# Performance work log

Measured on AMD Instinct MI355X. Metric: run time of the kernel, lower is better.

## Reference

```python
import jax, jax.numpy as jnp
import numpy as np

D = 128   # d_model
K = 128   # knn neighbors
NL = 4    # point transformer layers
EPS = 1e-5


def _timestep_embedding(t, dim):
    half = dim // 2
    freqs = jnp.exp(-jnp.log(10000.0) * jnp.arange(half, dtype=jnp.float32) / (half - 1))
    args = t.astype(jnp.float32)[:, None] * freqs[None, :]          # [B, half]
    return jnp.concatenate([jnp.sin(args), jnp.cos(args)], axis=-1)  # [B, dim]


def _layernorm(x, g, b):
    m = jnp.mean(x, axis=-1, keepdims=True)
    v = jnp.mean((x - m) ** 2, axis=-1, keepdims=True)
    return (x - m) / jnp.sqrt(v + EPS) * g + b


def _pt_layer(xyz, feat, Wq, bq, Wk, bk, Wv, bv, Wp1, bp1, Wp2, bp2, gamma, Wpr, bpr):
    # full pairwise squared distance [B,N,N]
    sq = jnp.sum(xyz * xyz, axis=-1)
    dist = sq[:, :, None] + sq[:, None, :] - 2.0 * jnp.einsum('bnd,bmd->bnm', xyz, xyz)
    _, idx = jax.lax.top_k(-dist, K)                 # k smallest -> [B,N,K]
    gather = jax.vmap(lambda p, i: p[i])             # per-batch gather along N
    nxyz = gather(xyz, idx)                          # [B,N,K,3]
    nfeat = gather(feat, idx)                        # [B,N,K,D]
    q = (feat @ Wq + bq)[:, :, None, :]              # [B,N,1,D]
    k = nfeat @ Wk + bk                              # [B,N,K,D]
    v = nfeat @ Wv + bv                              # [B,N,K,D]
    rel = xyz[:, :, None, :] - nxyz                  # [B,N,K,3]
    pe = jax.nn.relu(rel @ Wp1 + bp1) @ Wp2 + bp2    # [B,N,K,D]
    attn = jax.nn.softmax(jnp.sum(q - k + pe, axis=-1, keepdims=True), axis=-2)  # over K
    agg = jnp.sum(attn * (v + pe), axis=2)           # [B,N,D]
    return feat + gamma * (agg @ Wpr + bpr)


def reference(xyz, feat, x_t, t,
              pt_Wq, pt_bq, pt_Wk, pt_bk, pt_Wv, pt_bv,
              pt_Wp1, pt_bp1, pt_Wp2, pt_bp2, pt_gamma, pt_Wproj, pt_bproj,
              tW1, tb1, tW2, tb2,
              nW1, nb1, ng1, nbeta1, nW2, nb2, ng2, nbeta2, nW3, nb3):
    fused = feat
    for i in range(NL):
        fused = _pt_layer(xyz, fused,
                          pt_Wq[i], pt_bq[i], pt_Wk[i], pt_bk[i], pt_Wv[i], pt_bv[i],
                          pt_Wp1[i], pt_bp1[i], pt_Wp2[i], pt_bp2[i],
                          pt_gamma[i], pt_Wproj[i], pt_bproj[i])
    # DDPM head
    temb = _timestep_embedding(t, D)                 # [B,D]
    temb = jax.nn.relu(temb @ tW1 + tb1) @ tW2 + tb2
    temb = jnp.broadcast_to(temb[:, None, :], fused.shape[:2] + (D,))
    h = jnp.concatenate([x_t, fused, temb], axis=-1)  # [B,N,3+2D]
    h = jax.nn.relu(_layernorm(h @ nW1 + nb1, ng1, nbeta1))
    h = jax.nn.relu(_layernorm(h @ nW2 + nb2, ng2, nbeta2))
    return h @ nW3 + nb3                              # [B,N,3]


def setup_inputs() -> dict:
    key = jax.random.key(0)
    ks = jax.random.split(key, 32)
    B, N = 2, 2048
    rn = lambda k, shape, s=0.02: (jax.random.normal(k, shape) * s).astype(jnp.float32)
    in_dim = 3 + D + D
    return {
        'xyz': jax.random.normal(ks[0], (B, N, 3), dtype=jnp.float32),
        'feat': jax.random.normal(ks[1], (B, N, D), dtype=jnp.float32),
        'x_t': jax.random.normal(ks[2], (B, N, 3), dtype=jnp.float32),
        't': jax.random.randint(ks[3], (B,), 0, 1000),
        'pt_Wq': rn(ks[4], (NL, D, D)), 'pt_bq': jnp.zeros((NL, D), jnp.float32),
        'pt_Wk': rn(ks[5], (NL, D, D)), 'pt_bk': jnp.zeros((NL, D), jnp.float32),
        'pt_Wv': rn(ks[6], (NL, D, D)), 'pt_bv': jnp.zeros((NL, D), jnp.float32),
        'pt_Wp1': rn(ks[7], (NL, 3, D)), 'pt_bp1': jnp.zeros((NL, D), jnp.float32),
        'pt_Wp2': rn(ks[8], (NL, D, D)), 'pt_bp2': jnp.zeros((NL, D), jnp.float32),
        'pt_gamma': rn(ks[9], (NL,), 0.1),
        'pt_Wproj': rn(ks[10], (NL, D, D)), 'pt_bproj': jnp.zeros((NL, D), jnp.float32),
        'tW1': rn(ks[11], (D, D)), 'tb1': jnp.zeros((D,), jnp.float32),
        'tW2': rn(ks[12], (D, D)), 'tb2': jnp.zeros((D,), jnp.float32),
        'nW1': rn(ks[13], (in_dim, D)), 'nb1': jnp.zeros((D,), jnp.float32),
        'ng1': jnp.ones((D,), jnp.float32), 'nbeta1': jnp.zeros((D,), jnp.float32),
        'nW2': rn(ks[14], (D, D)), 'nb2': jnp.zeros((D,), jnp.float32),
        'ng2': jnp.ones((D,), jnp.float32), 'nbeta2': jnp.zeros((D,), jnp.float32),
        'nW3': rn(ks[15], (D, 3)), 'nb3': jnp.zeros((3,), jnp.float32),
    }
```

## Files before the change

### kernel.cpp

```cpp
#include <hip/hip_runtime.h>
#include <math.h>

#define B_SZ 2
#define N_PTS 2048
#define DM 128
#define KNN 128
#define NLAYER 4
#define ROWS (B_SZ * N_PTS)
#define RBV 4
#define EPSLN 1e-5f

__device__ __forceinline__ float waveSum(float v) {
#pragma unroll
  for (int o = 32; o > 0; o >>= 1) v += __shfl_xor(v, o, 64);
  return v;
}
__device__ __forceinline__ float waveMax(float v) {
#pragma unroll
  for (int o = 32; o > 0; o >>= 1) v = fmaxf(v, __shfl_xor(v, o, 64));
  return v;
}
__device__ __forceinline__ float blockSum128(float v, float* s2, int t) {
  float w = waveSum(v);
  __syncthreads();
  if ((t & 63) == 0) s2[t >> 6] = w;
  __syncthreads();
  return s2[0] + s2[1];
}
__device__ __forceinline__ unsigned waveScanIncl(unsigned v, int lane) {
#pragma unroll
  for (int o = 1; o < 64; o <<= 1) {
    unsigned u = (unsigned)__shfl_up((int)v, o, 64);
    if (lane >= o) v += u;
  }
  return v;
}

__global__ __launch_bounds__(256) void knn_kernel(const float* __restrict__ xyz,
                                                  int* __restrict__ idx) {
  int row = blockIdx.x;
  int b = row >> 11, i = row & (N_PTS - 1);
  const float* xb = xyz + (size_t)b * N_PTS * 3;
  int tid = threadIdx.x;
  int lane = tid & 63, wid = tid >> 6;

  __shared__ unsigned hist[256];
  __shared__ unsigned wred[4];
  __shared__ unsigned sel[2];

  float xi = xb[i * 3 + 0], yi = xb[i * 3 + 1], zi = xb[i * 3 + 2];
  float sqi = xi * xi + yi * yi + zi * zi;

  float p[24];
  {
    const float4* xb4 = (const float4*)xb;
#pragma unroll
    for (int q = 0; q < 6; ++q) {
      float4 v = xb4[tid * 6 + q];
      p[q * 4 + 0] = v.x; p[q * 4 + 1] = v.y; p[q * 4 + 2] = v.z; p[q * 4 + 3] = v.w;
    }
  }
  unsigned key[8];
#pragma unroll
  for (int s = 0; s < 8; ++s) {
    float xj = p[s * 3 + 0], yj = p[s * 3 + 1], zj = p[s * 3 + 2];
    float d = sqi + xj * xj + yj * yj + zj * zj -
              2.0f * (xi * xj + yi * yj + zi * zj);
    unsigned u = __float_as_uint(d);
    key[s] = (u & 0x80000000u) ? ~u : (u | 0x80000000u);
  }

  unsigned prefix = 0;
  unsigned need = KNN;
  for (int shift = 24; shift >= 0; shift -= 8) {
    hist[tid] = 0;
    __syncthreads();
    if (shift == 24) {
#pragma unroll
      for (int s = 0; s < 8; ++s) {
        unsigned bin = key[s] >> 24;
        unsigned long long act = __ballot(1);
        while (act) {
          int src = __builtin_ctzll(act);
          unsigned bsel = (unsigned)__shfl((int)bin, src, 64);
          unsigned long long grp = __ballot(bin == bsel);
          if (lane == src)
            atomicAdd(&hist[bsel], (unsigned)__builtin_popcountll(grp));
          act &= ~grp;
        }
      }
    } else {
#pragma unroll
      for (int s = 0; s < 8; ++s) {
        unsigned k = key[s];
        if ((k >> (shift + 8)) == prefix)
          atomicAdd(&hist[(k >> shift) & 255u], 1u);
      }
    }
    __syncthreads();
    unsigned h = hist[tid];
    unsigned incl = waveScanIncl(h, lane);
    if (lane == 63) wred[wid] = incl;
    __syncthreads();
    unsigned offs = 0;
    for (int w = 0; w < wid; ++w) offs += wred[w];
    incl += offs;
    unsigned excl = incl - h;
    if (excl < need && need <= incl) { sel[0] = (unsigned)tid; sel[1] = need - excl; }
    __syncthreads();
    prefix = (prefix << 8) | sel[0];
    need = sel[1];
  }
  unsigned T = prefix;
  int need_eq = (int)need;

  unsigned clt = 0, ceq = 0;
#pragma unroll
  for (int s = 0; s < 8; ++s) {
    clt += (key[s] < T);
    ceq += (key[s] == T);
  }
  unsigned packed = clt | (ceq << 16);
  unsigned incl = waveScanIncl(packed, lane);
  if (lane == 63) wred[wid] = incl;
  __syncthreads();
  unsigned offs = 0;
  for (int w = 0; w < wid; ++w) offs += wred[w];
  unsigned totAll = wred[0] + wred[1] + wred[2] + wred[3];
  incl += offs;
  unsigned excl = incl - packed;
  int lt_base = (int)(excl & 0xFFFFu);
  int eq_base = (int)(excl >> 16);
  int total_lt = (int)(totAll & 0xFFFFu);

  int* orow = idx + (size_t)row * KNN;
  int lpos = 0, epos = 0;
#pragma unroll
  for (int s = 0; s < 8; ++s) {
    int j = tid * 8 + s;
    unsigned k = key[s];
    if (k < T) {
      orow[lt_base + lpos] = j; lpos++;
    } else if (k == T) {
      int r = eq_base + epos; epos++;
      if (r < need_eq) orow[total_lt + r] = j;
    }
  }
}

__global__ __launch_bounds__(128) void prep_kernel(
    const float* __restrict__ Wq, const float* __restrict__ bq,
    const float* __restrict__ Wk, const float* __restrict__ bk,
    const float* __restrict__ Wp2, const float* __restrict__ bp2,
    float* __restrict__ rs, float* __restrict__ ssum,
    const int* __restrict__ t, const float* __restrict__ tW1,
    const float* __restrict__ tb1, const float* __restrict__ tW2,
    const float* __restrict__ tb2, float* __restrict__ temb) {
  int blk = blockIdx.x, d = threadIdx.x;
  __shared__ float s2[2];
  __shared__ float emb[DM];
  __shared__ float h1[DM];
  if (blk < NLAYER) {
    int l = blk;
    const float* wq = Wq + (size_t)l * DM * DM;
    const float* wk = Wk + (size_t)l * DM * DM;
    const float* wp2 = Wp2 + (size_t)l * DM * DM;
    float a = 0.f, b = 0.f, c = 0.f;
    for (int j = 0; j < DM; ++j) {
      a += wq[d * DM + j];
      b += wk[d * DM + j];
      c += wp2[d * DM + j];
    }
    rs[l * 3 * DM + d] = a;
    rs[l * 3 * DM + DM + d] = b;
    rs[l * 3 * DM + 2 * DM + d] = c;
    float sq = blockSum128(bq[l * DM + d], s2, d);
    float sk = blockSum128(bk[l * DM + d], s2, d);
    float sp = blockSum128(bp2[l * DM + d], s2, d);
    if (d == 0) { ssum[l * 4 + 0] = sq; ssum[l * 4 + 1] = sk; ssum[l * 4 + 2] = sp; }
  } else {
    int b = blk - NLAYER;
    float tv = (float)t[b];
    float lg = logf(10000.0f);
    if (d < 64) {
      float f = expf(-lg * (float)d / 63.0f);
      emb[d] = sinf(tv * f);
    } else {
      float f = expf(-lg * (float)(d - 64) / 63.0f);
      emb[d] = cosf(tv * f);
    }
    __syncthreads();
    float acc = tb1[d];
    for (int j = 0; j < DM; ++j) acc = fmaf(emb[j], tW1[j * DM + d], acc);
    h1[d] = fmaxf(acc, 0.f);
    __syncthreads();
    float acc2 = tb2[d];
    for (int j = 0; j < DM; ++j) acc2 = fmaf(h1[j], tW2[j * DM + d], acc2);
    temb[b * DM + d] = acc2;
  }
}

__global__ __launch_bounds__(256) void vqk_kernel(
    const float* __restrict__ feat, const float* __restrict__ Wv,
    const float* __restrict__ bv, const float* __restrict__ rs,
    const float* __restrict__ ssum, float* __restrict__ Vf,
    float* __restrict__ qsum, float* __restrict__ ksum) {
  int n0 = blockIdx.x * RBV;
  int t = threadIdx.x;
  int d = t & 127, half = t >> 7;
  __shared__ float fr[RBV][DM];
  __shared__ float part[RBV][DM];
  __shared__ float sA[2][RBV];
  __shared__ float sB[2][RBV];
#pragma unroll
  for (int u = 0; u < 2; ++u) {
    int r = half * 2 + u;
    fr[r][d] = feat[(size_t)(n0 + r) * DM + d];
  }
  __syncthreads();
  float acc[RBV] = {0.f, 0.f, 0.f, 0.f};
  int j0 = half * 64;
  for (int jj = 0; jj < 64; jj += 4) {
    int j = j0 + jj;
    float w0 = Wv[(j + 0) * DM + d], w1 = Wv[(j + 1) * DM + d];
    float w2 = Wv[(j + 2) * DM + d], w3 = Wv[(j + 3) * DM + d];
#pragma unroll
    for (int r = 0; r < RBV; ++r) {
      float4 f = *(const float4*)&fr[r][j];
      acc[r] = fmaf(f.x, w0, fmaf(f.y, w1, fmaf(f.z, w2, fmaf(f.w, w3, acc[r]))));
    }
  }
  if (half == 1) {
#pragma unroll
    for (int r = 0; r < RBV; ++r) part[r][d] = acc[r];
  }
  __syncthreads();
  if (half == 0) {
    float bvd = bv[d];
#pragma unroll
    for (int r = 0; r < RBV; ++r)
      Vf[(size_t)(n0 + r) * DM + d] = acc[r] + part[r][d] + bvd;
    int lane = t & 63, wid = (t >> 6) & 1;
    float rsq = rs[d], rsk = rs[DM + d];
#pragma unroll
    for (int r = 0; r < RBV; ++r) {
      float f = fr[r][d];
      float a = waveSum(f * rsq);
      float k = waveSum(f * rsk);
      if (lane == 0) { sA[wid][r] = a; sB[wid][r] = k; }
    }
  }
  __syncthreads();
  if (t < RBV) qsum[n0 + t] = sA[0][t] + sA[1][t] + ssum[0];
  if (t >= 64 && t < 64 + RBV) {
    int r = t - 64;
    ksum[n0 + r] = sB[0][r] + sB[1][r] + ssum[1];
  }
}

template <int LAST>
__global__ __launch_bounds__(256, 4) void fused_layer_kernel(
    const float* __restrict__ xyz, const int* __restrict__ idx,
    const float* __restrict__ fin, const float* __restrict__ Vf_in,
    const float* __restrict__ qsum_in, const float* __restrict__ ksum_in,
    const float* __restrict__ Wp1, const float* __restrict__ bp1,
    const float* __restrict__ rsL, const float* __restrict__ ssL,
    const float* __restrict__ Wp2, const float* __restrict__ bp2,
    const float* __restrict__ Wproj, const float* __restrict__ bproj,
    const float* __restrict__ gamma, int l, float* __restrict__ fout,
    const float* __restrict__ Wv_n, const float* __restrict__ bv_n,
    const float* __restrict__ rs_n, const float* __restrict__ ss_n,
    float* __restrict__ Vf_out, float* __restrict__ qsum_out,
    float* __restrict__ ksum_out,
    const float* __restrict__ x_t, const float* __restrict__ temb,
    const float* __restrict__ nW1, const float* __restrict__ nb1,
    const float* __restrict__ ng1, const float* __restrict__ nbe1,
    const float* __restrict__ nW2, const float* __restrict__ nb2,
    const float* __restrict__ ng2, const float* __restrict__ nbe2,
    const float* __restrict__ nW3, const float* __restrict__ nb3,
    float* __restrict__ out) {
  int n0 = blockIdx.x * 2;
  int t = threadIdx.x;
  int r = t >> 7, u = t & 127;
  int w = t >> 6, lane = t & 63;
  int b = n0 >> 11;
  int row = n0 + r;
  int d = u;

  __shared__ float4 rel4[2][KNN];
  __shared__ int joff[2][KNN];
  __shared__ float hrow[2][DM];
  __shared__ float zz[2][DM];
  __shared__ float part[2][2][DM];
  __shared__ float sred1[4];
  __shared__ float sred2[4];

  const float* xb = xyz + (size_t)b * N_PTS * 3;
  {
    int k = u;
    int i = row & (N_PTS - 1);
    float xi = xb[i * 3 + 0], yi = xb[i * 3 + 1], zi = xb[i * 3 + 2];
    int j = idx[(size_t)row * KNN + k];
    float rx = xi - xb[j * 3 + 0];
    float ry = yi - xb[j * 3 + 1];
    float rz = zi - xb[j * 3 + 2];

    const float4* W1x = (const float4*)Wp1;
    const float4* W1y = (const float4*)(Wp1 + DM);
    const float4* W1z = (const float4*)(Wp1 + 2 * DM);
    const float4* Bp = (const float4*)bp1;
    const float4* W2 = (const float4*)(rsL + 2 * DM);
    float acc0 = 0.f, acc1 = 0.f;
#pragma unroll 4
    for (int q = 0; q < DM / 4; q += 2) {
      float4 ax = W1x[q], ay = W1y[q], az = W1z[q], ab = Bp[q], c = W2[q];
      float h0v = fmaxf(fmaf(rx, ax.x, fmaf(ry, ay.x, fmaf(rz, az.x, ab.x))), 0.f);
      float h1v = fmaxf(fmaf(rx, ax.y, fmaf(ry, ay.y, fmaf(rz, az.y, ab.y))), 0.f);
      float h2v = fmaxf(fmaf(rx, ax.z, fmaf(ry, ay.z, fmaf(rz, az.z, ab.z))), 0.f);
      float h3v = fmaxf(fmaf(rx, ax.w, fmaf(ry, ay.w, fmaf(rz, az.w, ab.w))), 0.f);
      acc0 = fmaf(h0v, c.x, fmaf(h1v, c.y, fmaf(h2v, c.z, fmaf(h3v, c.w, acc0))));
      float4 ax2 = W1x[q + 1], ay2 = W1y[q + 1], az2 = W1z[q + 1],
             ab2 = Bp[q + 1], c2 = W2[q + 1];
      float h4 = fmaxf(fmaf(rx, ax2.x, fmaf(ry, ay2.x, fmaf(rz, az2.x, ab2.x))), 0.f);
      float h5 = fmaxf(fmaf(rx, ax2.y, fmaf(ry, ay2.y, fmaf(rz, az2.y, ab2.y))), 0.f);
      float h6 = fmaxf(fmaf(rx, ax2.z, fmaf(ry, ay2.z, fmaf(rz, az2.z, ab2.z))), 0.f);
      float h7 = fmaxf(fmaf(rx, ax2.w, fmaf(ry, ay2.w, fmaf(rz, az2.w, ab2.w))), 0.f);
      acc1 = fmaf(h4, c2.x, fmaf(h5, c2.y, fmaf(h6, c2.z, fmaf(h7, c2.w, acc1))));
    }
    float logit = qsum_in[row] - ksum_in[b * N_PTS + j] + (acc0 + acc1) + ssL[2];

    float m = waveMax(logit);
    if (lane == 0) sred1[w] = m;
    __syncthreads();
    m = fmaxf(sred1[r * 2], sred1[r * 2 + 1]);
    float e = __expf(logit - m);
    float sw = waveSum(e);
    if (lane == 0) sred2[w] = sw;
    __syncthreads();
    float ssm = sred2[r * 2] + sred2[r * 2 + 1];
    rel4[r][k] = make_float4(rx, ry, rz, e / ssm);
    joff[r][k] = j * (DM * 4);
  }
  __syncthreads();

  {
    float wdx = Wp1[d], wdy = Wp1[DM + d], wdz = Wp1[2 * DM + d], wdw = bp1[d];
    const char* vb = (const char*)(Vf_in + (size_t)b * N_PTS * DM + d);
    float ha0 = 0.f, ha1 = 0.f, va0 = 0.f, va1 = 0.f;
#pragma unroll 4
    for (int k = 0; k < KNN; k += 2) {
      float4 ra = rel4[r][k];
      float4 rb = rel4[r][k + 1];
      int ja = joff[r][k], jb = joff[r][k + 1];
      float Va = *(const float*)(vb + ja);
      float Vb = *(const float*)(vb + jb);
      float hA = fmaxf(fmaf(ra.x, wdx, fmaf(ra.y, wdy, fmaf(ra.z, wdz, wdw))), 0.f);
      float hB = fmaxf(fmaf(rb.x, wdx, fmaf(rb.y, wdy, fmaf(rb.z, wdz, wdw))), 0.f);
      ha0 = fmaf(ra.w, hA, ha0);
      ha1 = fmaf(rb.w, hB, ha1);
      va0 = fmaf(ra.w, Va, va0);
      va1 = fmaf(rb.w, Vb, va1);
    }
    hrow[r][d] = ha0 + ha1;
    zz[r][d] = va0 + va1;
  }
  __syncthreads();

  {
    float a0 = 0.f, a1 = 0.f;
    int j0 = r * 64;
    for (int jj = 0; jj < 64; jj += 4) {
      int j = j0 + jj;
      float w0 = Wp2[(j + 0) * DM + d], w1 = Wp2[(j + 1) * DM + d];
      float w2 = Wp2[(j + 2) * DM + d], w3 = Wp2[(j + 3) * DM + d];
      float4 f0 = *(const float4*)&hrow[0][j];
      float4 f1 = *(const float4*)&hrow[1][j];
      a0 = fmaf(f0.x, w0, fmaf(f0.y, w1, fmaf(f0.z, w2, fmaf(f0.w, w3, a0))));
      a1 = fmaf(f1.x, w0, fmaf(f1.y, w1, fmaf(f1.z, w2, fmaf(f1.w, w3, a1))));
    }
    part[r][0][d] = a0; part[r][1][d] = a1;
  }
  __syncthreads();
  zz[r][d] += part[0][r][d] + part[1][r][d] + bp2[d];
  __syncthreads();

  {
    float a0 = 0.f, a1 = 0.f;
    int j0 = r * 64;
    for (int jj = 0; jj < 64; jj += 4) {
      int j = j0 + jj;
      float w0 = Wproj[(j + 0) * DM + d], w1 = Wproj[(j + 1) * DM + d];
      float w2 = Wproj[(j + 2) * DM + d], w3 = Wproj[(j + 3) * DM + d];
      float4 f0 = *(const float4*)&zz[0][j];
      float4 f1 = *(const float4*)&zz[1][j];
      a0 = fmaf(f0.x, w0, fmaf(f0.y, w1, fmaf(f0.z, w2, fmaf(f0.w, w3, a0))));
      a1 = fmaf(f1.x, w0, fmaf(f1.y, w1, fmaf(f1.z, w2, fmaf(f1.w, w3, a1))));
    }
    part[r][0][d] = a0; part[r][1][d] = a1;
  }
  __syncthreads();
  float fo;
  {
    float s = part[0][r][d] + part[1][r][d] + bproj[d];
    fo = fin[(size_t)row * DM + d] + gamma[l] * s;
    if (!LAST) fout[(size_t)row * DM + d] = fo;
    hrow[r][d] = fo;
  }
  __syncthreads();

  if constexpr (!LAST) {
    {
      float qp = waveSum(fo * rs_n[d]);
      float kp = waveSum(fo * rs_n[DM + d]);
      if (lane == 0) { sred1[w] = qp; sred2[w] = kp; }
    }
    {
      float a0 = 0.f, a1 = 0.f;
      int j0 = r * 64;
      for (int jj = 0; jj < 64; jj += 4) {
        int j = j0 + jj;
        float w0 = Wv_n[(j + 0) * DM + d], w1 = Wv_n[(j + 1) * DM + d];
        float w2 = Wv_n[(j + 2) * DM + d], w3 = Wv_n[(j + 3) * DM + d];
        float4 f0 = *(const float4*)&hrow[0][j];
        float4 f1 = *(const float4*)&hrow[1][j];
        a0 = fmaf(f0.x, w0, fmaf(f0.y, w1, fmaf(f0.z, w2, fmaf(f0.w, w3, a0))));
        a1 = fmaf(f1.x, w0, fmaf(f1.y, w1, fmaf(f1.z, w2, fmaf(f1.w, w3, a1))));
      }
      part[r][0][d] = a0; part[r][1][d] = a1;
    }
    __syncthreads();
    Vf_out[(size_t)row * DM + d] = part[0][r][d] + part[1][r][d] + bv_n[d];
    if (u == 0) qsum_out[row] = sred1[r * 2] + sred1[r * 2 + 1] + ss_n[0];
    if (u == 1) ksum_out[row] = sred2[r * 2] + sred2[r * 2 + 1] + ss_n[1];
  } else {
    __shared__ float h0s[2][260];
    __shared__ float souts[4][3];
    h0s[r][3 + d] = hrow[r][d];
    h0s[r][131 + d] = temb[b * DM + d];
    if (d < 3) h0s[r][d] = x_t[(size_t)row * 3 + d];
    if (d == 0) h0s[r][259] = 0.f;
    __syncthreads();

    {
      float a0 = 0.f, a1 = 0.f;
      int j0 = r * 128;
      for (int jj = 0; jj < 128; jj += 4) {
        int j = j0 + jj;
        float w0 = nW1[(j + 0) * DM + d], w1 = nW1[(j + 1) * DM + d];
        float w2 = nW1[(j + 2) * DM + d], w3 = nW1[(j + 3) * DM + d];
        float4 f0 = *(const float4*)&h0s[0][j];
        float4 f1 = *(const float4*)&h0s[1][j];
        a0 = fmaf(f0.x, w0, fmaf(f0.y, w1, fmaf(f0.z, w2, fmaf(f0.w, w3, a0))));
        a1 = fmaf(f1.x, w0, fmaf(f1.y, w1, fmaf(f1.z, w2, fmaf(f1.w, w3, a1))));
      }
      if (r == 1) {
        for (int j = 256; j < 259; ++j) {
          float wv = nW1[j * DM + d];
          a0 = fmaf(h0s[0][j], wv, a0);
          a1 = fmaf(h0s[1][j], wv, a1);
        }
      }
      part[r][0][d] = a0; part[r][1][d] = a1;
    }
    __syncthreads();
    float acc1v = nb1[d] + part[0][r][d] + part[1][r][d];
    {
      float s1 = waveSum(acc1v), sq = waveSum(acc1v * acc1v);
      if (lane == 0) { sred1[w] = s1; sred2[w] = sq; }
      __syncthreads();
      float sx = sred1[r * 2] + sred1[r * 2 + 1];
      float sqq = sred2[r * 2] + sred2[r * 2 + 1];
      float m = sx * (1.0f / 128.0f);
      float var = sqq * (1.0f / 128.0f) - m * m;
      float y = (acc1v - m) * rsqrtf(var + EPSLN) * ng1[d] + nbe1[d];
      zz[r][d] = fmaxf(y, 0.f);
    }
    __syncthreads();
    {
      float a0 = 0.f, a1 = 0.f;
      int j0 = r * 64;
      for (int jj = 0; jj < 64; jj += 4) {
        int j = j0 + jj;
        float w0 = nW2[(j + 0) * DM + d], w1 = nW2[(j + 1) * DM + d];
        float w2 = nW2[(j + 2) * DM + d], w3 = nW2[(j + 3) * DM + d];
        float4 f0 = *(const float4*)&zz[0][j];
        float4 f1 = *(const float4*)&zz[1][j];
        a0 = fmaf(f0.x, w0, fmaf(f0.y, w1, fmaf(f0.z, w2, fmaf(f0.w, w3, a0))));
        a1 = fmaf(f1.x, w0, fmaf(f1.y, w1, fmaf(f1.z, w2, fmaf(f1.w, w3, a1))));
      }
      part[r][0][d] = a0; part[r][1][d] = a1;
    }
    __syncthreads();
    float acc2v = nb2[d] + part[0][r][d] + part[1][r][d];
    {
      float s1 = waveSum(acc2v), sq = waveSum(acc2v * acc2v);
      if (lane == 0) { sred1[w] = s1; sred2[w] = sq; }
      __syncthreads();
      float sx = sred1[r * 2] + sred1[r * 2 + 1];
      float sqq = sred2[r * 2] + sred2[r * 2 + 1];
      float m = sx * (1.0f / 128.0f);
      float var = sqq * (1.0f / 128.0f) - m * m;
      float y = (acc2v - m) * rsqrtf(var + EPSLN) * ng2[d] + nbe2[d];
      float y2 = fmaxf(y, 0.f);
      float p0 = waveSum(y2 * nW3[d * 3 + 0]);
      float p1 = waveSum(y2 * nW3[d * 3 + 1]);
      float p2 = waveSum(y2 * nW3[d * 3 + 2]);
      if (lane == 0) { souts[w][0] = p0; souts[w][1] = p1; souts[w][2] = p2; }
    }
    __syncthreads();
    if (u < 3)
      out[(size_t)row * 3 + u] =
          souts[r * 2][u] + souts[r * 2 + 1][u] + nb3[u];
  }
}

extern "C" void kernel_launch(void* const* d_in, const int* in_sizes, int n_in,
                              void* d_out, int out_size, void* d_ws,
                              size_t ws_size, hipStream_t stream) {
  const float* xyz = (const float*)d_in[0];
  const float* feat = (const float*)d_in[1];
  const float* x_t = (const float*)d_in[2];
  const int* t = (const int*)d_in[3];
  const float* Wq = (const float*)d_in[4];
  const float* bq = (const float*)d_in[5];
  const float* Wk = (const float*)d_in[6];
  const float* bk = (const float*)d_in[7];
  const float* Wv = (const float*)d_in[8];
  const float* bv = (const float*)d_in[9];
  const float* Wp1 = (const float*)d_in[10];
  const float* bp1 = (const float*)d_in[11];
  const float* Wp2 = (const float*)d_in[12];
  const float* bp2 = (const float*)d_in[13];
  const float* gamma = (const float*)d_in[14];
  const float* Wproj = (const float*)d_in[15];
  const float* bproj = (const float*)d_in[16];
  const float* tW1 = (const float*)d_in[17];
  const float* tb1 = (const float*)d_in[18];
  const float* tW2 = (const float*)d_in[19];
  const float* tb2 = (const float*)d_in[20];
  const float* nW1 = (const float*)d_in[21];
  const float* nb1 = (const float*)d_in[22];
  const float* ng1 = (const float*)d_in[23];
  const float* nbe1 = (const float*)d_in[24];
  const float* nW2 = (const float*)d_in[25];
  const float* nb2 = (const float*)d_in[26];
  const float* ng2 = (const float*)d_in[27];
  const float* nbe2 = (const float*)d_in[28];
  const float* nW3 = (const float*)d_in[29];
  const float* nb3 = (const float*)d_in[30];
  float* out = (float*)d_out;

  char* ws = (char*)d_ws;
  size_t off = 0;
  int* w_idx = (int*)(ws + off); off += (size_t)ROWS * KNN * 4;
  float* w_VfA = (float*)(ws + off); off += (size_t)ROWS * DM * 4;
  float* w_VfB = (float*)(ws + off); off += (size_t)ROWS * DM * 4;
  float* w_qsA = (float*)(ws + off); off += (size_t)ROWS * 4;
  float* w_ksA = (float*)(ws + off); off += (size_t)ROWS * 4;
  float* w_qsB = (float*)(ws + off); off += (size_t)ROWS * 4;
  float* w_ksB = (float*)(ws + off); off += (size_t)ROWS * 4;
  float* w_fA = (float*)(ws + off); off += (size_t)ROWS * DM * 4;
  float* w_fB = (float*)(ws + off); off += (size_t)ROWS * DM * 4;
  float* w_temb = (float*)(ws + off); off += (size_t)B_SZ * DM * 4;
  float* w_rs = (float*)(ws + off); off += (size_t)NLAYER * 3 * DM * 4;
  float* w_ssum = (float*)(ws + off); off += (size_t)NLAYER * 4 * 4;

  knn_kernel<<<ROWS, 256, 0, stream>>>(xyz, w_idx);
  prep_kernel<<<NLAYER + B_SZ, 128, 0, stream>>>(Wq, bq, Wk, bk, Wp2, bp2,
                                                 w_rs, w_ssum, t, tW1, tb1,
                                                 tW2, tb2, w_temb);
  vqk_kernel<<<ROWS / RBV, 256, 0, stream>>>(feat, Wv, bv, w_rs, w_ssum,
                                             w_VfA, w_qsA, w_ksA);

  const float* fins[4] = {feat, w_fA, w_fB, w_fA};
  float* fouts[4] = {w_fA, w_fB, w_fA, w_fB};
  const float* VfIn[4] = {w_VfA, w_VfB, w_VfA, w_VfB};
  float* VfOut[4] = {w_VfB, w_VfA, w_VfB, w_VfA};
  const float* qsIn[4] = {w_qsA, w_qsB, w_qsA, w_qsB};
  float* qsOut[4] = {w_qsB, w_qsA, w_qsB, w_qsA};
  const float* ksIn[4] = {w_ksA, w_ksB, w_ksA, w_ksB};
  float* ksOut[4] = {w_ksB, w_ksA, w_ksB, w_ksA};

  for (int l = 0; l < NLAYER; ++l) {
    const float* rsL = w_rs + (size_t)l * 3 * DM;
    const float* ssL = w_ssum + (size_t)l * 4;
    int ln = (l + 1 < NLAYER) ? (l + 1) : l;
    const float* rsN = w_rs + (size_t)ln * 3 * DM;
    const float* ssN = w_ssum + (size_t)ln * 4;
    if (l < NLAYER - 1) {
      fused_layer_kernel<0><<<ROWS / 2, 256, 0, stream>>>(
          xyz, w_idx, fins[l], VfIn[l], qsIn[l], ksIn[l],
          Wp1 + (size_t)l * 3 * DM, bp1 + (size_t)l * DM, rsL, ssL,
          Wp2 + (size_t)l * DM * DM, bp2 + (size_t)l * DM,
          Wproj + (size_t)l * DM * DM, bproj + (size_t)l * DM, gamma, l,
          fouts[l], Wv + (size_t)ln * DM * DM, bv + (size_t)ln * DM, rsN, ssN,
          VfOut[l], qsOut[l], ksOut[l], x_t, w_temb, nW1, nb1, ng1, nbe1, nW2,
          nb2, ng2, nbe2, nW3, nb3, out);
    } else {
      fused_layer_kernel<1><<<ROWS / 2, 256, 0, stream>>>(
          xyz, w_idx, fins[l], VfIn[l], qsIn[l], ksIn[l],
          Wp1 + (size_t)l * 3 * DM, bp1 + (size_t)l * DM, rsL, ssL,
          Wp2 + (size_t)l * DM * DM, bp2 + (size_t)l * DM,
          Wproj + (size_t)l * DM * DM, bproj + (size_t)l * DM, gamma, l,
          fouts[l], Wv + (size_t)ln * DM * DM, bv + (size_t)ln * DM, rsN, ssN,
          VfOut[l], qsOut[l], ksOut[l], x_t, w_temb, nW1, nb1, ng1, nbe1, nW2,
          nb2, ng2, nbe2, nW3, nb3, out);
    }
  }
}
```

Before: 229.5 us.

## Process eight rows per block with wave-per-row softmax and 8-row GEMVs

The fused layer kernel now handles eight query rows per 512-thread block instead of two rows per 256-thread block. Each wave owns one row for the neighbor logits and softmax, so the reduction needs only wave shuffles and no block syncs. The dense 128x128 matvecs (Wp2, Wproj, Wv, and the head MLP) are rewritten as 8-row GEMVs, so each weight load is reused across eight rows and partial sums are combined through shared memory. In exchange the block uses more shared memory and more registers per thread, which may reduce occupancy, and the grid has fewer blocks.

```diff
diff --git a/kernel.cpp b/kernel.cpp
--- a/kernel.cpp
+++ b/kernel.cpp
@@ -8,6 +8,7 @@
 #define NLAYER 4
 #define ROWS (B_SZ * N_PTS)
 #define RBV 4
+#define RB8 8
 #define EPSLN 1e-5f
 
 __device__ __forceinline__ float waveSum(float v) {
@@ -34,6 +35,21 @@
     if (lane >= o) v += u;
   }
   return v;
+}
+
+template <int STRIDE>
+__device__ __forceinline__ void gemv8(const float* src, const float* W, int j0,
+                                      int cnt, int d, float* a) {
+  for (int jj = 0; jj < cnt; jj += 4) {
+    int j = j0 + jj;
+    float w0 = W[(j + 0) * DM + d], w1 = W[(j + 1) * DM + d];
+    float w2 = W[(j + 2) * DM + d], w3 = W[(j + 3) * DM + d];
+#pragma unroll
+    for (int rr = 0; rr < 8; ++rr) {
+      float4 f = *(const float4*)(src + rr * STRIDE + j);
+      a[rr] = fmaf(f.x, w0, fmaf(f.y, w1, fmaf(f.z, w2, fmaf(f.w, w3, a[rr]))));
+    }
+  }
 }
 
 __global__ __launch_bounds__(256) void knn_kernel(const float* __restrict__ xyz,
@@ -259,7 +275,7 @@
 }
 
 template <int LAST>
-__global__ __launch_bounds__(256, 4) void fused_layer_kernel(
+__global__ __launch_bounds__(512, 4) void fused_layer_kernel(
     const float* __restrict__ xyz, const int* __restrict__ idx,
     const float* __restrict__ fin, const float* __restrict__ Vf_in,
     const float* __restrict__ qsum_in, const float* __restrict__ ksum_in,
@@ -279,238 +295,263 @@
     const float* __restrict__ ng2, const float* __restrict__ nbe2,
     const float* __restrict__ nW3, const float* __restrict__ nb3,
     float* __restrict__ out) {
-  int n0 = blockIdx.x * 2;
+  int n0 = blockIdx.x * RB8;
   int t = threadIdx.x;
-  int r = t >> 7, u = t & 127;
   int w = t >> 6, lane = t & 63;
+  int q = t >> 7, d = t & 127;
   int b = n0 >> 11;
-  int row = n0 + r;
-  int d = u;
-
-  __shared__ float4 rel4[2][KNN];
-  __shared__ int joff[2][KNN];
-  __shared__ float hrow[2][DM];
-  __shared__ float zz[2][DM];
-  __shared__ float part[2][2][DM];
-  __shared__ float sred1[4];
-  __shared__ float sred2[4];
+
+  __shared__ float4 rel4[RB8][KNN];
+  __shared__ int joff[RB8][KNN];
+  __shared__ float hrow[RB8][DM];
+  __shared__ float zz[RB8][DM];
+  float* part = (float*)rel4;
 
   const float* xb = xyz + (size_t)b * N_PTS * 3;
+
   {
-    int k = u;
+    int row = n0 + w;
     int i = row & (N_PTS - 1);
     float xi = xb[i * 3 + 0], yi = xb[i * 3 + 1], zi = xb[i * 3 + 2];
-    int j = idx[(size_t)row * KNN + k];
-    float rx = xi - xb[j * 3 + 0];
-    float ry = yi - xb[j * 3 + 1];
-    float rz = zi - xb[j * 3 + 2];
+    int j1 = idx[(size_t)row * KNN + lane];
+    int j2 = idx[(size_t)row * KNN + lane + 64];
+    float rx1 = xi - xb[j1 * 3 + 0], ry1 = yi - xb[j1 * 3 + 1], rz1 = zi - xb[j1 * 3 + 2];
+    float rx2 = xi - xb[j2 * 3 + 0], ry2 = yi - xb[j2 * 3 + 1], rz2 = zi - xb[j2 * 3 + 2];
 
     const float4* W1x = (const float4*)Wp1;
     const float4* W1y = (const float4*)(Wp1 + DM);
     const float4* W1z = (const float4*)(Wp1 + 2 * DM);
     const float4* Bp = (const float4*)bp1;
     const float4* W2 = (const float4*)(rsL + 2 * DM);
-    float acc0 = 0.f, acc1 = 0.f;
-#pragma unroll 4
-    for (int q = 0; q < DM / 4; q += 2) {
-      float4 ax = W1x[q], ay = W1y[q], az = W1z[q], ab = Bp[q], c = W2[q];
-      float h0v = fmaxf(fmaf(rx, ax.x, fmaf(ry, ay.x, fmaf(rz, az.x, ab.x))), 0.f);
-      float h1v = fmaxf(fmaf(rx, ax.y, fmaf(ry, ay.y, fmaf(rz, az.y, ab.y))), 0.f);
-      float h2v = fmaxf(fmaf(rx, ax.z, fmaf(ry, ay.z, fmaf(rz, az.z, ab.z))), 0.f);
-      float h3v = fmaxf(fmaf(rx, ax.w, fmaf(ry, ay.w, fmaf(rz, az.w, ab.w))), 0.f);
-      acc0 = fmaf(h0v, c.x, fmaf(h1v, c.y, fmaf(h2v, c.z, fmaf(h3v, c.w, acc0))));
-      float4 ax2 = W1x[q + 1], ay2 = W1y[q + 1], az2 = W1z[q + 1],
-             ab2 = Bp[q + 1], c2 = W2[q + 1];
-      float h4 = fmaxf(fmaf(rx, ax2.x, fmaf(ry, ay2.x, fmaf(rz, az2.x, ab2.x))), 0.f);
-      float h5 = fmaxf(fmaf(rx, ax2.y, fmaf(ry, ay2.y, fmaf(rz, az2.y, ab2.y))), 0.f);
-      float h6 = fmaxf(fmaf(rx, ax2.z, fmaf(ry, ay2.z, fmaf(rz, az2.z, ab2.z))), 0.f);
-      float h7 = fmaxf(fmaf(rx, ax2.w, fmaf(ry, ay2.w, fmaf(rz, az2.w, ab2.w))), 0.f);
-      acc1 = fmaf(h4, c2.x, fmaf(h5, c2.y, fmaf(h6, c2.z, fmaf(h7, c2.w, acc1))));
-    }
-    float logit = qsum_in[row] - ksum_in[b * N_PTS + j] + (acc0 + acc1) + ssL[2];
-
-    float m = waveMax(logit);
-    if (lane == 0) sred1[w] = m;
-    __syncthreads();
-    m = fmaxf(sred1[r * 2], sred1[r * 2 + 1]);
-    float e = __expf(logit - m);
-    float sw = waveSum(e);
-    if (lane == 0) sred2[w] = sw;
-    __syncthreads();
-    float ssm = sred2[r * 2] + sred2[r * 2 + 1];
-    rel4[r][k] = make_float4(rx, ry, rz, e / ssm);
-    joff[r][k] = j * (DM * 4);
+    float acc1 = 0.f, acc2 = 0.f;
+#pragma unroll 8
+    for (int qq = 0; qq < DM / 4; ++qq) {
+      float4 ax = W1x[qq], ay = W1y[qq], az = W1z[qq], ab = Bp[qq], c = W2[qq];
+      float hA = fmaxf(fmaf(rx1, ax.x, fmaf(ry1, ay.x, fmaf(rz1, az.x, ab.x))), 0.f);
+      float hB = fmaxf(fmaf(rx1, ax.y, fmaf(ry1, ay.y, fmaf(rz1, az.y, ab.y))), 0.f);
+      float hC = fmaxf(fmaf(rx1, ax.z, fmaf(ry1, ay.z, fmaf(rz1, az.z, ab.z))), 0.f);
+      float hD = fmaxf(fmaf(rx1, ax.w, fmaf(ry1, ay.w, fmaf(rz1, az.w, ab.w))), 0.f);
+      acc1 = fmaf(hA, c.x, fmaf(hB, c.y, fmaf(hC, c.z, fmaf(hD, c.w, acc1))));
+      float hE = fmaxf(fmaf(rx2, ax.x, fmaf(ry2, ay.x, fmaf(rz2, az.x, ab.x))), 0.f);
+      float hF = fmaxf(fmaf(rx2, ax.y, fmaf(ry2, ay.y, fmaf(rz2, az.y, ab.y))), 0.f);
+      float hG = fmaxf(fmaf(rx2, ax.z, fmaf(ry2, ay.z, fmaf(rz2, az.z, ab.z))), 0.f);
+      float hH = fmaxf(fmaf(rx2, ax.w, fmaf(ry2, ay.w, fmaf(rz2, az.w, ab.w))), 0.f);
+      acc2 = fmaf(hE, c.x, fmaf(hF, c.y, fmaf(hG, c.z, fmaf(hH, c.w, acc2))));
+    }
+    float qs = qsum_in[row] + ssL[2];
+    float l1 = qs - ksum_in[b * N_PTS + j1] + acc1;
+    float l2 = qs - ksum_in[b * N_PTS + j2] + acc2;
+    float m = waveMax(fmaxf(l1, l2));
+    float e1 = __expf(l1 - m), e2 = __expf(l2 - m);
+    float s = waveSum(e1 + e2);
+    float inv = 1.0f / s;
+    rel4[w][lane] = make_float4(rx1, ry1, rz1, e1 * inv);
+    rel4[w][lane + 64] = make_float4(rx2, ry2, rz2, e2 * inv);
+    joff[w][lane] = j1 * (DM * 4);
+    joff[w][lane + 64] = j2 * (DM * 4);
   }
   __syncthreads();
 
   {
-    float wdx = Wp1[d], wdy = Wp1[DM + d], wdz = Wp1[2 * DM + d], wdw = bp1[d];
-    const char* vb = (const char*)(Vf_in + (size_t)b * N_PTS * DM + d);
-    float ha0 = 0.f, ha1 = 0.f, va0 = 0.f, va1 = 0.f;
+    int d1 = lane, d2 = lane + 64;
+    float wx1 = Wp1[d1], wy1 = Wp1[DM + d1], wz1 = Wp1[2 * DM + d1], wb1 = bp1[d1];
+    float wx2 = Wp1[d2], wy2 = Wp1[DM + d2], wz2 = Wp1[2 * DM + d2], wb2 = bp1[d2];
+    const char* vbase = (const char*)(Vf_in + (size_t)b * N_PTS * DM);
+    const char* v1 = vbase + (size_t)d1 * 4;
+    const char* v2 = vbase + (size_t)d2 * 4;
+    float ha1a = 0.f, ha1b = 0.f, ha2a = 0.f, ha2b = 0.f;
+    float va1a = 0.f, va1b = 0.f, va2a = 0.f, va2b = 0.f;
 #pragma unroll 4
     for (int k = 0; k < KNN; k += 2) {
-      float4 ra = rel4[r][k];
-      float4 rb = rel4[r][k + 1];
-      int ja = joff[r][k], jb = joff[r][k + 1];
-      float Va = *(const float*)(vb + ja);
-      float Vb = *(const float*)(vb + jb);
-      float hA = fmaxf(fmaf(ra.x, wdx, fmaf(ra.y, wdy, fmaf(ra.z, wdz, wdw))), 0.f);
-      float hB = fmaxf(fmaf(rb.x, wdx, fmaf(rb.y, wdy, fmaf(rb.z, wdz, wdw))), 0.f);
-      ha0 = fmaf(ra.w, hA, ha0);
-      ha1 = fmaf(rb.w, hB, ha1);
-      va0 = fmaf(ra.w, Va, va0);
-      va1 = fmaf(rb.w, Vb, va1);
-    }
-    hrow[r][d] = ha0 + ha1;
-    zz[r][d] = va0 + va1;
+      float4 ra = rel4[w][k];
+      float4 rb = rel4[w][k + 1];
+      int ja = joff[w][k], jb = joff[w][k + 1];
+      float Va1 = *(const float*)(v1 + ja);
+      float Vb1 = *(const float*)(v1 + jb);
+      float Va2 = *(const float*)(v2 + ja);
+      float Vb2 = *(const float*)(v2 + jb);
+      float hA1 = fmaxf(fmaf(ra.x, wx1, fmaf(ra.y, wy1, fmaf(ra.z, wz1, wb1))), 0.f);
+      float hB1 = fmaxf(fmaf(rb.x, wx1, fmaf(rb.y, wy1, fmaf(rb.z, wz1, wb1))), 0.f);
+      float hA2 = fmaxf(fmaf(ra.x, wx2, fmaf(ra.y, wy2, fmaf(ra.z, wz2, wb2))), 0.f);
+      float hB2 = fmaxf(fmaf(rb.x, wx2, fmaf(rb.y, wy2, fmaf(rb.z, wz2, wb2))), 0.f);
+      ha1a = fmaf(ra.w, hA1, ha1a);
+      ha1b = fmaf(rb.w, hB1, ha1b);
+      ha2a = fmaf(ra.w, hA2, ha2a);
+      ha2b = fmaf(rb.w, hB2, ha2b);
+      va1a = fmaf(ra.w, Va1, va1a);
+      va1b = fmaf(rb.w, Vb1, va1b);
+      va2a = fmaf(ra.w, Va2, va2a);
+      va2b = fmaf(rb.w, Vb2, va2b);
+    }
+    hrow[w][d1] = ha1a + ha1b;
+    hrow[w][d2] = ha2a + ha2b;
+    zz[w][d1] = va1a + va1b;
+    zz[w][d2] = va2a + va2b;
   }
   __syncthreads();
 
   {
-    float a0 = 0.f, a1 = 0.f;
-    int j0 = r * 64;
-    for (int jj = 0; jj < 64; jj += 4) {
-      int j = j0 + jj;
-      float w0 = Wp2[(j + 0) * DM + d], w1 = Wp2[(j + 1) * DM + d];
-      float w2 = Wp2[(j + 2) * DM + d], w3 = Wp2[(j + 3) * DM + d];
-      float4 f0 = *(const float4*)&hrow[0][j];
-      float4 f1 = *(const float4*)&hrow[1][j];
-      a0 = fmaf(f0.x, w0, fmaf(f0.y, w1, fmaf(f0.z, w2, fmaf(f0.w, w3, a0))));
-      a1 = fmaf(f1.x, w0, fmaf(f1.y, w1, fmaf(f1.z, w2, fmaf(f1.w, w3, a1))));
-    }
-    part[r][0][d] = a0; part[r][1][d] = a1;
-  }
-  __syncthreads();
-  zz[r][d] += part[0][r][d] + part[1][r][d] + bp2[d];
-  __syncthreads();
-
+    float a[RB8] = {0.f, 0.f, 0.f, 0.f, 0.f, 0.f, 0.f, 0.f};
+    gemv8<DM>(&hrow[0][0], Wp2, q * 32, 32, d, a);
+    float* pq = part + (q * RB8) * DM + d;
+#pragma unroll
+    for (int rr = 0; rr < RB8; ++rr) pq[rr * DM] = a[rr];
+  }
+  __syncthreads();
   {
-    float a0 = 0.f, a1 = 0.f;
-    int j0 = r * 64;
-    for (int jj = 0; jj < 64; jj += 4) {
-      int j = j0 + jj;
-      float w0 = Wproj[(j + 0) * DM + d], w1 = Wproj[(j + 1) * DM + d];
-      float w2 = Wproj[(j + 2) * DM + d], w3 = Wproj[(j + 3) * DM + d];
-      float4 f0 = *(const float4*)&zz[0][j];
-      float4 f1 = *(const float4*)&zz[1][j];
-      a0 = fmaf(f0.x, w0, fmaf(f0.y, w1, fmaf(f0.z, w2, fmaf(f0.w, w3, a0))));
-      a1 = fmaf(f1.x, w0, fmaf(f1.y, w1, fmaf(f1.z, w2, fmaf(f1.w, w3, a1))));
-    }
-    part[r][0][d] = a0; part[r][1][d] = a1;
-  }
-  __syncthreads();
-  float fo;
+    int r0 = q * 2, r1 = q * 2 + 1;
+    float bpd = bp2[d];
+    zz[r0][d] += part[(0 * RB8 + r0) * DM + d] + part[(1 * RB8 + r0) * DM + d] +
+                 part[(2 * RB8 + r0) * DM + d] + part[(3 * RB8 + r0) * DM + d] + bpd;
+    zz[r1][d] += part[(0 * RB8 + r1) * DM + d] + part[(1 * RB8 + r1) * DM + d] +
+                 part[(2 * RB8 + r1) * DM + d] + part[(3 * RB8 + r1) * DM + d] + bpd;
+  }
+  __syncthreads();
+
   {
-    float s = part[0][r][d] + part[1][r][d] + bproj[d];
-    fo = fin[(size_t)row * DM + d] + gamma[l] * s;
-    if (!LAST) fout[(size_t)row * DM + d] = fo;
-    hrow[r][d] = fo;
+    float a[RB8] = {0.f, 0.f, 0.f, 0.f, 0.f, 0.f, 0.f, 0.f};
+    gemv8<DM>(&zz[0][0], Wproj, q * 32, 32, d, a);
+    float* pq = part + (q * RB8) * DM + d;
+#pragma unroll
+    for (int rr = 0; rr < RB8; ++rr) pq[rr * DM] = a[rr];
+  }
+  __syncthreads();
+  {
+    int r0 = q * 2, r1 = q * 2 + 1;
+    float g = gamma[l];
+    float bpr = bproj[d];
+    float s0 = part[(0 * RB8 + r0) * DM + d] + part[(1 * RB8 + r0) * DM + d] +
+               part[(2 * RB8 + r0) * DM + d] + part[(3 * RB8 + r0) * DM + d] + bpr;
+    float s1 = part[(0 * RB8 + r1) * DM + d] + part[(1 * RB8 + r1) * DM + d] +
+               part[(2 * RB8 + r1) * DM + d] + part[(3 * RB8 + r1) * DM + d] + bpr;
+    float fo0 = fin[(size_t)(n0 + r0) * DM + d] + g * s0;
+    float fo1 = fin[(size_t)(n0 + r1) * DM + d] + g * s1;
+    if (!LAST) {
+      fout[(size_t)(n0 + r0) * DM + d] = fo0;
+      fout[(size_t)(n0 + r1) * DM + d] = fo1;
+    }
+    hrow[r0][d] = fo0;
+    hrow[r1][d] = fo1;
   }
   __syncthreads();
 
   if constexpr (!LAST) {
     {
-      float qp = waveSum(fo * rs_n[d]);
-      float kp = waveSum(fo * rs_n[DM + d]);
-      if (lane == 0) { sred1[w] = qp; sred2[w] = kp; }
-    }
-    {
-      float a0 = 0.f, a1 = 0.f;
-      int j0 = r * 64;
-      for (int jj = 0; jj < 64; jj += 4) {
-        int j = j0 + jj;
-        float w0 = Wv_n[(j + 0) * DM + d], w1 = Wv_n[(j + 1) * DM + d];
-        float w2 = Wv_n[(j + 2) * DM + d], w3 = Wv_n[(j + 3) * DM + d];
-        float4 f0 = *(const float4*)&hrow[0][j];
-        float4 f1 = *(const float4*)&hrow[1][j];
-        a0 = fmaf(f0.x, w0, fmaf(f0.y, w1, fmaf(f0.z, w2, fmaf(f0.w, w3, a0))));
-        a1 = fmaf(f1.x, w0, fmaf(f1.y, w1, fmaf(f1.z, w2, fmaf(f1.w, w3, a1))));
+      int d1 = lane, d2 = lane + 64;
+      float fo1 = hrow[w][d1], fo2 = hrow[w][d2];
+      float qp = waveSum(fo1 * rs_n[d1] + fo2 * rs_n[d2]);
+      float kp = waveSum(fo1 * rs_n[DM + d1] + fo2 * rs_n[DM + d2]);
+      if (lane == 0) {
+        qsum_out[n0 + w] = qp + ss_n[0];
+        ksum_out[n0 + w] = kp + ss_n[1];
       }
-      part[r][0][d] = a0; part[r][1][d] = a1;
-    }
-    __syncthreads();
-    Vf_out[(size_t)row * DM + d] = part[0][r][d] + part[1][r][d] + bv_n[d];
-    if (u == 0) qsum_out[row] = sred1[r * 2] + sred1[r * 2 + 1] + ss_n[0];
-    if (u == 1) ksum_out[row] = sred2[r * 2] + sred2[r * 2 + 1] + ss_n[1];
+    }
+    {
+      float a[RB8] = {0.f, 0.f, 0.f, 0.f, 0.f, 0.f, 0.f, 0.f};
+      gemv8<DM>(&hrow[0][0], Wv_n, q * 32, 32, d, a);
+      float* pq = part + (q * RB8) * DM + d;
+#pragma unroll
+      for (int rr = 0; rr < RB8; ++rr) pq[rr * DM] = a[rr];
+    }
+    __syncthreads();
+    {
+      int r0 = q * 2, r1 = q * 2 + 1;
+      float bvd = bv_n[d];
+      Vf_out[(size_t)(n0 + r0) * DM + d] =
+          part[(0 * RB8 + r0) * DM + d] + part[(1 * RB8 + r0) * DM + d] +
+          part[(2 * RB8 + r0) * DM + d] + part[(3 * RB8 + r0) * DM + d] + bvd;
+      Vf_out[(size_t)(n0 + r1) * DM + d] =
+          part[(0 * RB8 + r1) * DM + d] + part[(1 * RB8 + r1) * DM + d] +
+          part[(2 * RB8 + r1) * DM + d] + part[(3 * RB8 + r1) * DM + d] + bvd;
+    }
   } else {
-    __shared__ float h0s[2][260];
-    __shared__ float souts[4][3];
-    h0s[r][3 + d] = hrow[r][d];
-    h0s[r][131 + d] = temb[b * DM + d];
-    if (d < 3) h0s[r][d] = x_t[(size_t)row * 3 + d];
-    if (d == 0) h0s[r][259] = 0.f;
-    __syncthreads();
-
-    {
-      float a0 = 0.f, a1 = 0.f;
-      int j0 = r * 128;
-      for (int jj = 0; jj < 128; jj += 4) {
-        int j = j0 + jj;
-        float w0 = nW1[(j + 0) * DM + d], w1 = nW1[(j + 1) * DM + d];
-        float w2 = nW1[(j + 2) * DM + d], w3 = nW1[(j + 3) * DM + d];
-        float4 f0 = *(const float4*)&h0s[0][j];
-        float4 f1 = *(const float4*)&h0s[1][j];
-        a0 = fmaf(f0.x, w0, fmaf(f0.y, w1, fmaf(f0.z, w2, fmaf(f0.w, w3, a0))));
-        a1 = fmaf(f1.x, w0, fmaf(f1.y, w1, fmaf(f1.z, w2, fmaf(f1.w, w3, a1))));
+    __shared__ float h0s[RB8][260];
+    {
+      int r0 = q * 2, r1 = q * 2 + 1;
+#pragma unroll
+      for (int rr = r0; rr <= r1; ++rr) {
+        h0s[rr][3 + d] = hrow[rr][d];
+        h0s[rr][131 + d] = temb[b * DM + d];
+        if (d < 3) h0s[rr][d] = x_t[(size_t)(n0 + rr) * 3 + d];
+        if (d == 0) h0s[rr][259] = 0.f;
       }
-      if (r == 1) {
+    }
+    __syncthreads();
+
+    {
+      float a[RB8] = {0.f, 0.f, 0.f, 0.f, 0.f, 0.f, 0.f, 0.f};
+      gemv8<260>(&h0s[0][0], nW1, q * 64, 64, d, a);
+      if (q == 3) {
         for (int j = 256; j < 259; ++j) {
           float wv = nW1[j * DM + d];
-          a0 = fmaf(h0s[0][j], wv, a0);
-          a1 = fmaf(h0s[1][j], wv, a1);
+#pragma unroll
+          for (int rr = 0; rr < RB8; ++rr) a[rr] = fmaf(h0s[rr][j], wv, a[rr]);
         }
       }
-      part[r][0][d] = a0; part[r][1][d] = a1;
-    }
-    __syncthreads();
-    float acc1v = nb1[d] + part[0][r][d] + part[1][r][d];
-    {
-      float s1 = waveSum(acc1v), sq = waveSum(acc1v * acc1v);
-      if (lane == 0) { sred1[w] = s1; sred2[w] = sq; }
-      __syncthreads();
-      float sx = sred1[r * 2] + sred1[r * 2 + 1];
-      float sqq = sred2[r * 2] + sred2[r * 2 + 1];
-      float m = sx * (1.0f / 128.0f);
-      float var = sqq * (1.0f / 128.0f) - m * m;
-      float y = (acc1v - m) * rsqrtf(var + EPSLN) * ng1[d] + nbe1[d];
-      zz[r][d] = fmaxf(y, 0.f);
-    }
-    __syncthreads();
-    {
-      float a0 = 0.f, a1 = 0.f;
-      int j0 = r * 64;
-      for (int jj = 0; jj < 64; jj += 4) {
-        int j = j0 + jj;
-        float w0 = nW2[(j + 0) * DM + d], w1 = nW2[(j + 1) * DM + d];
-        float w2 = nW2[(j + 2) * DM + d], w3 = nW2[(j + 3) * DM + d];
-        float4 f0 = *(const float4*)&zz[0][j];
-        float4 f1 = *(const float4*)&zz[1][j];
-        a0 = fmaf(f0.x, w0, fmaf(f0.y, w1, fmaf(f0.z, w2, fmaf(f0.w, w3, a0))));
-        a1 = fmaf(f1.x, w0, fmaf(f1.y, w1, fmaf(f1.z, w2, fmaf(f1.w, w3, a1))));
+      float* pq = part + (q * RB8) * DM + d;
+#pragma unroll
+      for (int rr = 0; rr < RB8; ++rr) pq[rr * DM] = a[rr];
+    }
+    __syncthreads();
+    {
+      int r0 = q * 2, r1 = q * 2 + 1;
+      float nb = nb1[d];
+      zz[r0][d] = nb + part[(0 * RB8 + r0) * DM + d] + part[(1 * RB8 + r0) * DM + d] +
+                  part[(2 * RB8 + r0) * DM + d] + part[(3 * RB8 + r0) * DM + d];
+      zz[r1][d] = nb + part[(0 * RB8 + r1) * DM + d] + part[(1 * RB8 + r1) * DM + d] +
+                  part[(2 * RB8 + r1) * DM + d] + part[(3 * RB8 + r1) * DM + d];
+    }
+    __syncthreads();
+    {
+      int d1 = lane, d2 = lane + 64;
+      float x1 = zz[w][d1], x2 = zz[w][d2];
+      float s1 = waveSum(x1 + x2);
+      float sq = waveSum(x1 * x1 + x2 * x2);
+      float m = s1 * (1.0f / 128.0f);
+      float var = sq * (1.0f / 128.0f) - m * m;
+      float rstd = rsqrtf(var + EPSLN);
+      float y1 = fmaxf((x1 - m) * rstd * ng1[d1] + nbe1[d1], 0.f);
+      float y2 = fmaxf((x2 - m) * rstd * ng1[d2] + nbe1[d2], 0.f);
+      zz[w][d1] = y1;
+      zz[w][d2] = y2;
+    }
+    __syncthreads();
+    {
+      float a[RB8] = {0.f, 0.f, 0.f, 0.f, 0.f, 0.f, 0.f, 0.f};
+      gemv8<DM>(&zz[0][0], nW2, q * 32, 32, d, a);
+      float* pq = part + (q * RB8) * DM + d;
+#pragma unroll
+      for (int rr = 0; rr < RB8; ++rr) pq[rr * DM] = a[rr];
+    }
+    __syncthreads();
+    {
+      int r0 = q * 2, r1 = q * 2 + 1;
+      float nb = nb2[d];
+      hrow[r0][d] = nb + part[(0 * RB8 + r0) * DM + d] + part[(1 * RB8 + r0) * DM + d] +
+                    part[(2 * RB8 + r0) * DM + d] + part[(3 * RB8 + r0) * DM + d];
+      hrow[r1][d] = nb + part[(0 * RB8 + r1) * DM + d] + part[(1 * RB8 + r1) * DM + d] +
+                    part[(2 * RB8 + r1) * DM + d] + part[(3 * RB8 + r1) * DM + d];
+    }
+    __syncthreads();
+    {
+      int d1 = lane, d2 = lane + 64;
+      float x1 = hrow[w][d1], x2 = hrow[w][d2];
+      float s1 = waveSum(x1 + x2);
+      float sq = waveSum(x1 * x1 + x2 * x2);
+      float m = s1 * (1.0f / 128.0f);
+      float var = sq * (1.0f / 128.0f) - m * m;
+      float rstd = rsqrtf(var + EPSLN);
+      float y1 = fmaxf((x1 - m) * rstd * ng2[d1] + nbe2[d1], 0.f);
+      float y2 = fmaxf((x2 - m) * rstd * ng2[d2] + nbe2[d2], 0.f);
+      float p0 = waveSum(y1 * nW3[d1 * 3 + 0] + y2 * nW3[d2 * 3 + 0]);
+      float p1 = waveSum(y1 * nW3[d1 * 3 + 1] + y2 * nW3[d2 * 3 + 1]);
+      float p2 = waveSum(y1 * nW3[d1 * 3 + 2] + y2 * nW3[d2 * 3 + 2]);
+      if (lane == 0) {
+        out[(size_t)(n0 + w) * 3 + 0] = p0 + nb3[0];
+        out[(size_t)(n0 + w) * 3 + 1] = p1 + nb3[1];
+        out[(size_t)(n0 + w) * 3 + 2] = p2 + nb3[2];
       }
-      part[r][0][d] = a0; part[r][1][d] = a1;
-    }
-    __syncthreads();
-    float acc2v = nb2[d] + part[0][r][d] + part[1][r][d];
-    {
-      float s1 = waveSum(acc2v), sq = waveSum(acc2v * acc2v);
-      if (lane == 0) { sred1[w] = s1; sred2[w] = sq; }
-      __syncthreads();
-      float sx = sred1[r * 2] + sred1[r * 2 + 1];
-      float sqq = sred2[r * 2] + sred2[r * 2 + 1];
-      float m = sx * (1.0f / 128.0f);
-      float var = sqq * (1.0f / 128.0f) - m * m;
-      float y = (acc2v - m) * rsqrtf(var + EPSLN) * ng2[d] + nbe2[d];
-      float y2 = fmaxf(y, 0.f);
-      float p0 = waveSum(y2 * nW3[d * 3 + 0]);
-      float p1 = waveSum(y2 * nW3[d * 3 + 1]);
-      float p2 = waveSum(y2 * nW3[d * 3 + 2]);
-      if (lane == 0) { souts[w][0] = p0; souts[w][1] = p1; souts[w][2] = p2; }
-    }
-    __syncthreads();
-    if (u < 3)
-      out[(size_t)row * 3 + u] =
-          souts[r * 2][u] + souts[r * 2 + 1][u] + nb3[u];
+    }
   }
 }
 
@@ -588,7 +629,7 @@
     const float* rsN = w_rs + (size_t)ln * 3 * DM;
     const float* ssN = w_ssum + (size_t)ln * 4;
     if (l < NLAYER - 1) {
-      fused_layer_kernel<0><<<ROWS / 2, 256, 0, stream>>>(
+      fused_layer_kernel<0><<<ROWS / RB8, 512, 0, stream>>>(
           xyz, w_idx, fins[l], VfIn[l], qsIn[l], ksIn[l],
           Wp1 + (size_t)l * 3 * DM, bp1 + (size_t)l * DM, rsL, ssL,
           Wp2 + (size_t)l * DM * DM, bp2 + (size_t)l * DM,
@@ -597,7 +638,7 @@
           VfOut[l], qsOut[l], ksOut[l], x_t, w_temb, nW1, nb1, ng1, nbe1, nW2,
           nb2, ng2, nbe2, nW3, nb3, out);
     } else {
-      fused_layer_kernel<1><<<ROWS / 2, 256, 0, stream>>>(
+      fused_layer_kernel<1><<<ROWS / RB8, 512, 0, stream>>>(
           xyz, w_idx, fins[l], VfIn[l], qsIn[l], ksIn[l],
           Wp1 + (size_t)l * 3 * DM, bp1 + (size_t)l * DM, rsL, ssL,
           Wp2 + (size_t)l * DM * DM, bp2 + (size_t)l * DM,
```

After: 194.7 us. 15.2% less time.
